# Kernel tuning notes

Measured on AMD Instinct MI355X. Metric: run time of the kernel, lower is better.

## Reference

```python
import jax, jax.numpy as jnp
import numpy as np

N_NODES = 50000
N_EDGES = 600000
IN_CH = 128
OUT_CH = 32
L1 = IN_CH - (IN_CH - OUT_CH) // 3          # 96
L2 = IN_CH - (2 * (IN_CH - OUT_CH)) // 3    # 64


def _lin(key, fan_in, fan_out):
    bound = 1.0 / np.sqrt(fan_in)
    return jax.random.uniform(key, (fan_in, fan_out), jnp.float32, -bound, bound)


def setup_inputs() -> dict:
    key = jax.random.key(0)
    ks = jax.random.split(key, 12)
    x = jax.random.normal(ks[0], (N_NODES, IN_CH), jnp.float32)
    edge_index = jax.random.randint(ks[1], (2, N_EDGES), 0, N_NODES, jnp.int64 if jax.config.jax_enable_x64 else jnp.int32)
    return {
        "x": x,
        "edge_index": edge_index,
        "w1_rel": _lin(ks[2], IN_CH, L1),
        "w1_root": _lin(ks[3], IN_CH, L1),
        "b1": jnp.zeros((L1,), jnp.float32),
        "w2_rel": _lin(ks[4], L1, L2),
        "w2_root": _lin(ks[5], L1, L2),
        "b2": jnp.zeros((L2,), jnp.float32),
        "w_mu": _lin(ks[6], L2, OUT_CH),
        "b_mu": jnp.zeros((OUT_CH,), jnp.float32),
        "w_ls": _lin(ks[7], L2, OUT_CH),
        "b_ls": jnp.zeros((OUT_CH,), jnp.float32),
    }


def reference(x, edge_index, w1_rel, w1_root, b1, w2_rel, w2_root, b2,
              w_mu, b_mu, w_ls, b_ls):
    src, dst = edge_index[0], edge_index[1]

    # PyG GraphConv (aggr='add'): out_i = W_rel @ sum_{j->i} x_j + W_root @ x_i + b
    def graph_conv(h, wr, wroot, b):
        agg = jax.ops.segment_sum(h[src], dst, num_segments=N_NODES)
        return agg @ wr + h @ wroot + b

    h = jax.nn.relu(graph_conv(x, w1_rel, w1_root, b1))
    h = jax.nn.relu(graph_conv(h, w2_rel, w2_root, b2))

    # GCNConv: add self-loops, symmetric deg^-1/2 normalization (shared by mu / logstd)
    loops = jnp.arange(N_NODES, dtype=src.dtype)
    src_sl = jnp.concatenate([src, loops])
    dst_sl = jnp.concatenate([dst, loops])
    deg = jax.ops.segment_sum(jnp.ones_like(dst_sl, h.dtype), dst_sl, num_segments=N_NODES)
    dinv = jnp.where(deg > 0, jax.lax.rsqrt(deg), 0.0)
    norm = dinv[src_sl] * dinv[dst_sl]  # [E+N]

    def gcn(h, w, b):
        m = (h @ w)[src_sl] * norm[:, None]
        return jax.ops.segment_sum(m, dst_sl, num_segments=N_NODES) + b

    return gcn(h, w_mu, b_mu), gcn(h, w_ls, b_ls)
```

## Files before the change

kernel.cpp:

```cpp
#include <hip/hip_runtime.h>
#include <cstddef>

static constexpr int NN = 50000;
static constexpr int NE = 600000;
static constexpr int NB = (NN + 255) / 256;

using f32x4 = __attribute__((ext_vector_type(4))) float;
using s16x8 = __attribute__((ext_vector_type(8))) short;

__device__ inline float bf2f(unsigned short u) {
    return __uint_as_float(((unsigned)u) << 16);
}
__device__ inline unsigned short f2bf(float f) {
    unsigned u = __float_as_uint(f);
    unsigned r = u + 0x7fffu + ((u >> 16) & 1u);
    return (unsigned short)(r >> 16);
}
__device__ inline float lof(unsigned u) { return __uint_as_float(u << 16); }
__device__ inline float hif(unsigned u) { return __uint_as_float(u & 0xffff0000u); }
__device__ inline unsigned packbf(float a, float b) {
    return (unsigned)f2bf(a) | ((unsigned)f2bf(b) << 16);
}

__global__ __launch_bounds__(256)
void zero_deg_k(int* __restrict__ deg) {
    int i = blockIdx.x * 256 + threadIdx.x;
    if (i < NN) deg[i] = 0;
}

__global__ __launch_bounds__(256)
void count_deg_k(const int* __restrict__ dstv, int* __restrict__ deg) {
    int e = blockIdx.x * 256 + threadIdx.x;
    if (e < NE) atomicAdd(&deg[dstv[e]], 1);
}

__global__ __launch_bounds__(256)
void scan_reduce_k(const int* __restrict__ deg, int* __restrict__ partial) {
    __shared__ int buf[256];
    int i = blockIdx.x * 256 + threadIdx.x;
    buf[threadIdx.x] = (i < NN) ? deg[i] : 0;
    __syncthreads();
    #pragma unroll
    for (int off = 128; off > 0; off >>= 1) {
        if (threadIdx.x < off) buf[threadIdx.x] += buf[threadIdx.x + off];
        __syncthreads();
    }
    if (threadIdx.x == 0) partial[blockIdx.x] = buf[0];
}

__global__ __launch_bounds__(256)
void scan_partials_k(int* __restrict__ partial, int* __restrict__ row_start) {
    __shared__ int buf[256];
    int t = threadIdx.x;
    int v = (t < NB) ? partial[t] : 0;
    buf[t] = v;
    __syncthreads();
    #pragma unroll
    for (int off = 1; off < 256; off <<= 1) {
        int tv = (t >= off) ? buf[t - off] : 0;
        __syncthreads();
        buf[t] += tv;
        __syncthreads();
    }
    if (t < NB) partial[t] = buf[t] - v;
    if (t == 255) row_start[NN] = buf[255];
}

__global__ __launch_bounds__(256)
void scan_final_k(const int* __restrict__ deg, const int* __restrict__ partial,
                  int* __restrict__ row_start, int* __restrict__ cursor,
                  float* __restrict__ dinv) {
    __shared__ int buf[256];
    int i = blockIdx.x * 256 + threadIdx.x;
    int t = threadIdx.x;
    int v = (i < NN) ? deg[i] : 0;
    buf[t] = v;
    __syncthreads();
    #pragma unroll
    for (int off = 1; off < 256; off <<= 1) {
        int tv = (t >= off) ? buf[t - off] : 0;
        __syncthreads();
        buf[t] += tv;
        __syncthreads();
    }
    if (i < NN) {
        int pos = partial[blockIdx.x] + buf[t] - v;
        row_start[i] = pos;
        cursor[i] = pos;
        dinv[i] = rsqrtf((float)v + 1.0f);
    }
}

__global__ __launch_bounds__(256)
void fill_k(const int* __restrict__ srcv, const int* __restrict__ dstv,
            int* __restrict__ cursor, int* __restrict__ csr)
{
    int e = blockIdx.x * 256 + threadIdx.x;
    if (e < NE) {
        int pos = atomicAdd(&cursor[dstv[e]], 1);
        csr[pos] = srcv[e];
    }
}

__global__ __launch_bounds__(256)
void wprep_k(const float* __restrict__ w1_rel, const float* __restrict__ w1_root,
             const float* __restrict__ w2_rel, const float* __restrict__ w2_root,
             const float* __restrict__ w_mu,   const float* __restrict__ w_ls,
             unsigned short* __restrict__ wt1, unsigned short* __restrict__ wt2,
             unsigned short* __restrict__ wt3)
{
    int i = blockIdx.x * 256 + threadIdx.x;
    if (i < 24576) {
        int k = i / 192, n = i % 192;
        float v = (n < 96) ? w1_rel[k * 96 + n] : w1_root[k * 96 + (n - 96)];
        wt1[n * 128 + k] = f2bf(v);
    } else if (i < 36864) {
        int j = i - 24576;
        int k = j / 128, n = j % 128;
        float v = (n < 64) ? w2_rel[k * 64 + n] : w2_root[k * 64 + (n - 64)];
        wt2[n * 96 + k] = f2bf(v);
    } else if (i < 40960) {
        int j = i - 36864;
        int k = j / 64, n = j % 64;
        float v = (n < 32) ? w_mu[k * 32 + n] : w_ls[k * 32 + (n - 32)];
        wt3[n * 64 + k] = f2bf(v);
    }
}

template<int K, int NH, bool XB, bool SCALE>
__global__ __launch_bounds__(256)
void gemm_mfma(const void* __restrict__ Xv,
               const unsigned short* __restrict__ WT,
               const float* __restrict__ biasB,
               const float* __restrict__ scale,
               unsigned short* __restrict__ out0,
               unsigned short* __restrict__ out1)
{
    constexpr int KQ = K / 4;
    constexpr int PB = K * 2;
    constexpr int KS = K / 32;
    constexpr int NT = NH / 16;
    __shared__ short lds[(128 + NH) * K];
    char* ldsb = (char*)lds;
    const int tid = threadIdx.x;
    const int blk = blockIdx.x;
    const int half = blockIdx.y;

    const unsigned short* wt = WT + (size_t)half * NH * K;
    unsigned short* outp = half ? out1 : out0;

    #pragma unroll
    for (int it = 0; it < KQ / 2; ++it) {
        int idx = it * 256 + tid;
        int r = idx / KQ, c4 = idx % KQ;
        int node = blk * 128 + r; if (node >= NN) node = NN - 1;
        uint2 p;
        if (XB) {
            p = *(const uint2*)((const unsigned short*)Xv + (size_t)node * K + c4 * 4);
        } else {
            float4 v = *(const float4*)((const float*)Xv + (size_t)node * K + c4 * 4);
            p.x = packbf(v.x, v.y); p.y = packbf(v.z, v.w);
        }
        unsigned byte = (unsigned)(r * PB + c4 * 8) ^ ((unsigned)(r & 7) << 4);
        *(uint2*)(ldsb + byte) = p;
    }
    #pragma unroll
    for (int it = 0; it < NH * KQ / 256; ++it) {
        int idx = it * 256 + tid;
        int n = idx / KQ, c4 = idx % KQ;
        uint2 p = *(const uint2*)(wt + (size_t)n * K + c4 * 4);
        int pr = 128 + n;
        unsigned byte = (unsigned)(pr * PB + c4 * 8) ^ ((unsigned)(pr & 7) << 4);
        *(uint2*)(ldsb + byte) = p;
    }
    __syncthreads();

    const int wv = tid >> 6, lane = tid & 63;
    const int r15 = lane & 15, g = lane >> 4;

    s16x8 afr[2][KS];
    #pragma unroll
    for (int ms = 0; ms < 2; ++ms) {
        #pragma unroll
        for (int ks = 0; ks < KS; ++ks) {
            int r = wv * 32 + ms * 16 + r15;
            unsigned byte = (unsigned)(r * PB + ks * 64 + g * 16) ^ ((unsigned)(r & 7) << 4);
            afr[ms][ks] = *(const s16x8*)(ldsb + byte);
        }
    }

    #pragma unroll
    for (int nt = 0; nt < NT; ++nt) {
        s16x8 bfr[KS];
        #pragma unroll
        for (int ks = 0; ks < KS; ++ks) {
            int pr = 128 + nt * 16 + r15;
            unsigned byte = (unsigned)(pr * PB + ks * 64 + g * 16) ^ ((unsigned)(pr & 7) << 4);
            bfr[ks] = *(const s16x8*)(ldsb + byte);
        }
        int c = nt * 16 + r15;
        float bias = (half && biasB) ? biasB[c] : 0.f;
        #pragma unroll
        for (int ms = 0; ms < 2; ++ms) {
            f32x4 acc = {0.f, 0.f, 0.f, 0.f};
            #pragma unroll
            for (int ks = 0; ks < KS; ++ks)
                acc = __builtin_amdgcn_mfma_f32_16x16x32_bf16(afr[ms][ks], bfr[ks], acc, 0, 0, 0);
            int nb = blk * 128 + wv * 32 + ms * 16 + g * 4;
            #pragma unroll
            for (int rg = 0; rg < 4; ++rg) {
                int node = nb + rg;
                if (node < NN) {
                    float v = acc[rg] + bias;
                    if (SCALE) v *= scale[node];
                    outp[(size_t)node * NH + c] = f2bf(v);
                }
            }
        }
    }
}

template<int OC>
__global__ __launch_bounds__(256)
void gather_relu_k(const int* __restrict__ row_start,
                   const int* __restrict__ csr,
                   const unsigned short* __restrict__ msg,
                   unsigned short* __restrict__ hio)
{
    constexpr int G = OC / 8;
    int idx = blockIdx.x * 256 + threadIdx.x;
    if (idx >= NN * G) return;
    int i  = idx / G;
    int c8 = (idx - i * G) * 8;
    const size_t ro = (size_t)i * OC + c8;
    float a[8];
    {
        uint4 h = *(const uint4*)&hio[ro];
        a[0] = lof(h.x); a[1] = hif(h.x); a[2] = lof(h.y); a[3] = hif(h.y);
        a[4] = lof(h.z); a[5] = hif(h.z); a[6] = lof(h.w); a[7] = hif(h.w);
    }
    int e0 = row_start[i], e1 = row_start[i + 1];
    int e = e0;
    for (; e + 2 <= e1; e += 2) {
        int s0 = csr[e], s1 = csr[e + 1];
        uint4 v0 = *(const uint4*)&msg[(size_t)s0 * OC + c8];
        uint4 v1 = *(const uint4*)&msg[(size_t)s1 * OC + c8];
        a[0] += lof(v0.x); a[1] += hif(v0.x); a[2] += lof(v0.y); a[3] += hif(v0.y);
        a[4] += lof(v0.z); a[5] += hif(v0.z); a[6] += lof(v0.w); a[7] += hif(v0.w);
        a[0] += lof(v1.x); a[1] += hif(v1.x); a[2] += lof(v1.y); a[3] += hif(v1.y);
        a[4] += lof(v1.z); a[5] += hif(v1.z); a[6] += lof(v1.w); a[7] += hif(v1.w);
    }
    if (e < e1) {
        int s = csr[e];
        uint4 v = *(const uint4*)&msg[(size_t)s * OC + c8];
        a[0] += lof(v.x); a[1] += hif(v.x); a[2] += lof(v.y); a[3] += hif(v.y);
        a[4] += lof(v.z); a[5] += hif(v.z); a[6] += lof(v.w); a[7] += hif(v.w);
    }
    uint4 o;
    o.x = packbf(fmaxf(a[0], 0.f), fmaxf(a[1], 0.f));
    o.y = packbf(fmaxf(a[2], 0.f), fmaxf(a[3], 0.f));
    o.z = packbf(fmaxf(a[4], 0.f), fmaxf(a[5], 0.f));
    o.w = packbf(fmaxf(a[6], 0.f), fmaxf(a[7], 0.f));
    *(uint4*)&hio[ro] = o;
}

__global__ __launch_bounds__(256)
void gather_gcn_k(const int* __restrict__ row_start,
                  const int* __restrict__ csr,
                  const unsigned short* __restrict__ y,
                  const float* __restrict__ dinv,
                  const float* __restrict__ b_mu,
                  const float* __restrict__ b_ls,
                  float* __restrict__ out)
{
    int idx = blockIdx.x * 256 + threadIdx.x;
    if (idx >= NN * 8) return;
    int i  = idx >> 3;
    int c8 = (idx & 7) * 8;
    float a[8];
    {
        uint4 h = *(const uint4*)&y[(size_t)i * 64 + c8];
        a[0] = lof(h.x); a[1] = hif(h.x); a[2] = lof(h.y); a[3] = hif(h.y);
        a[4] = lof(h.z); a[5] = hif(h.z); a[6] = lof(h.w); a[7] = hif(h.w);
    }
    int e0 = row_start[i], e1 = row_start[i + 1];
    int e = e0;
    for (; e + 2 <= e1; e += 2) {
        int s0 = csr[e], s1 = csr[e + 1];
        uint4 v0 = *(const uint4*)&y[(size_t)s0 * 64 + c8];
        uint4 v1 = *(const uint4*)&y[(size_t)s1 * 64 + c8];
        a[0] += lof(v0.x); a[1] += hif(v0.x); a[2] += lof(v0.y); a[3] += hif(v0.y);
        a[4] += lof(v0.z); a[5] += hif(v0.z); a[6] += lof(v0.w); a[7] += hif(v0.w);
        a[0] += lof(v1.x); a[1] += hif(v1.x); a[2] += lof(v1.y); a[3] += hif(v1.y);
        a[4] += lof(v1.z); a[5] += hif(v1.z); a[6] += lof(v1.w); a[7] += hif(v1.w);
    }
    if (e < e1) {
        int s = csr[e];
        uint4 v = *(const uint4*)&y[(size_t)s * 64 + c8];
        a[0] += lof(v.x); a[1] += hif(v.x); a[2] += lof(v.y); a[3] += hif(v.y);
        a[4] += lof(v.z); a[5] += hif(v.z); a[6] += lof(v.w); a[7] += hif(v.w);
    }
    float di = dinv[i];
    const float* b;
    float* o;
    if (c8 < 32) { b = &b_mu[c8];      o = &out[(size_t)i * 32 + c8]; }
    else         { b = &b_ls[c8 - 32]; o = &out[(size_t)NN * 32 + (size_t)i * 32 + (c8 - 32)]; }
    float4 r0, r1;
    r0.x = di * a[0] + b[0]; r0.y = di * a[1] + b[1];
    r0.z = di * a[2] + b[2]; r0.w = di * a[3] + b[3];
    r1.x = di * a[4] + b[4]; r1.y = di * a[5] + b[5];
    r1.z = di * a[6] + b[6]; r1.w = di * a[7] + b[7];
    *(float4*)&o[0] = r0;
    *(float4*)&o[4] = r1;
}

extern "C" void kernel_launch(void* const* d_in, const int* in_sizes, int n_in,
                              void* d_out, int out_size, void* d_ws, size_t ws_size,
                              hipStream_t stream)
{
    (void)in_sizes; (void)n_in; (void)out_size; (void)ws_size;
    const float* x       = (const float*)d_in[0];
    const int*   ei      = (const int*)d_in[1];
    const int*   srcv    = ei;
    const int*   dstv    = ei + NE;
    const float* w1_rel  = (const float*)d_in[2];
    const float* w1_root = (const float*)d_in[3];
    const float* b1      = (const float*)d_in[4];
    const float* w2_rel  = (const float*)d_in[5];
    const float* w2_root = (const float*)d_in[6];
    const float* b2      = (const float*)d_in[7];
    const float* w_mu    = (const float*)d_in[8];
    const float* b_mu    = (const float*)d_in[9];
    const float* w_ls    = (const float*)d_in[10];
    const float* b_ls    = (const float*)d_in[11];
    float* out = (float*)d_out;

    char* ws = (char*)d_ws;
    unsigned short* t1 = (unsigned short*)(ws);
    unsigned short* h1 = (unsigned short*)(ws + 9600000);
    unsigned short* t2 = (unsigned short*)(ws + 19200000);
    unsigned short* h2 = (unsigned short*)(ws + 25600000);
    unsigned short* y  = (unsigned short*)(ws + 32000000);
    int* csr       = (int*)(ws + 38400000);
    int* row_start = (int*)(ws + 40800000);
    int* cursor    = (int*)(ws + 41000016);
    float* dinv    = (float*)(ws + 41200016);
    int* deg       = (int*)(ws + 41400016);
    int* partial   = (int*)(ws + 41600016);
    unsigned short* wt1 = (unsigned short*)(ws + 41700016);
    unsigned short* wt2 = (unsigned short*)(ws + 41749168);
    unsigned short* wt3 = (unsigned short*)(ws + 41773744);

    zero_deg_k<<<NB, 256, 0, stream>>>(deg);
    wprep_k<<<160, 256, 0, stream>>>(w1_rel, w1_root, w2_rel, w2_root, w_mu, w_ls,
                                     wt1, wt2, wt3);
    count_deg_k<<<(NE + 255) / 256, 256, 0, stream>>>(dstv, deg);
    scan_reduce_k<<<NB, 256, 0, stream>>>(deg, partial);
    scan_partials_k<<<1, 256, 0, stream>>>(partial, row_start);
    scan_final_k<<<NB, 256, 0, stream>>>(deg, partial, row_start, cursor, dinv);
    fill_k<<<(NE + 255) / 256, 256, 0, stream>>>(srcv, dstv, cursor, csr);

    const int NGB = (NN + 127) / 128;

    gemm_mfma<128, 96, false, false><<<dim3(NGB, 2), 256, 0, stream>>>(
        x, wt1, b1, nullptr, t1, h1);
    gather_relu_k<96><<<(NN * 12 + 255) / 256, 256, 0, stream>>>(row_start, csr, t1, h1);

    gemm_mfma<96, 64, true, false><<<dim3(NGB, 2), 256, 0, stream>>>(
        h1, wt2, b2, nullptr, t2, h2);
    gather_relu_k<64><<<(NN * 8 + 255) / 256, 256, 0, stream>>>(row_start, csr, t2, h2);

    gemm_mfma<64, 64, true, true><<<dim3(NGB, 1), 256, 0, stream>>>(
        h2, wt3, nullptr, dinv, y, nullptr);
    gather_gcn_k<<<(NN * 8 + 255) / 256, 256, 0, stream>>>(row_start, csr, y, dinv, b_mu, b_ls, out);
}
```

Measured before the change: 178.6 us.

## Fuse neighbor gather+ReLU into following GEMM and merge preprocessing kernels

Each layer's CSR gather, root-term add and ReLU now runs inside the next layer's MFMA GEMM kernel. The activated 64-node tile is written straight to LDS instead of round-tripping h1/h2 through global memory, which removes two kernels and the intermediate writes and reads. The degree zeroing is merged with weight prep, and the partial-sum scan is folded into the final scan kernel, cutting launches. In exchange, the gather's irregular latency now sits inside the GEMM blocks, with fewer threads per node-feature and more LDS per block.

```diff
diff --git a/kernel.cpp b/kernel.cpp
--- a/kernel.cpp
+++ b/kernel.cpp
@@ -23,93 +23,15 @@
 }
 
 __global__ __launch_bounds__(256)
-void zero_deg_k(int* __restrict__ deg) {
+void zero_wprep_k(int* __restrict__ deg,
+                  const float* __restrict__ w1_rel, const float* __restrict__ w1_root,
+                  const float* __restrict__ w2_rel, const float* __restrict__ w2_root,
+                  const float* __restrict__ w_mu,   const float* __restrict__ w_ls,
+                  unsigned short* __restrict__ wt1, unsigned short* __restrict__ wt2,
+                  unsigned short* __restrict__ wt3)
+{
     int i = blockIdx.x * 256 + threadIdx.x;
     if (i < NN) deg[i] = 0;
-}
-
-__global__ __launch_bounds__(256)
-void count_deg_k(const int* __restrict__ dstv, int* __restrict__ deg) {
-    int e = blockIdx.x * 256 + threadIdx.x;
-    if (e < NE) atomicAdd(&deg[dstv[e]], 1);
-}
-
-__global__ __launch_bounds__(256)
-void scan_reduce_k(const int* __restrict__ deg, int* __restrict__ partial) {
-    __shared__ int buf[256];
-    int i = blockIdx.x * 256 + threadIdx.x;
-    buf[threadIdx.x] = (i < NN) ? deg[i] : 0;
-    __syncthreads();
-    #pragma unroll
-    for (int off = 128; off > 0; off >>= 1) {
-        if (threadIdx.x < off) buf[threadIdx.x] += buf[threadIdx.x + off];
-        __syncthreads();
-    }
-    if (threadIdx.x == 0) partial[blockIdx.x] = buf[0];
-}
-
-__global__ __launch_bounds__(256)
-void scan_partials_k(int* __restrict__ partial, int* __restrict__ row_start) {
-    __shared__ int buf[256];
-    int t = threadIdx.x;
-    int v = (t < NB) ? partial[t] : 0;
-    buf[t] = v;
-    __syncthreads();
-    #pragma unroll
-    for (int off = 1; off < 256; off <<= 1) {
-        int tv = (t >= off) ? buf[t - off] : 0;
-        __syncthreads();
-        buf[t] += tv;
-        __syncthreads();
-    }
-    if (t < NB) partial[t] = buf[t] - v;
-    if (t == 255) row_start[NN] = buf[255];
-}
-
-__global__ __launch_bounds__(256)
-void scan_final_k(const int* __restrict__ deg, const int* __restrict__ partial,
-                  int* __restrict__ row_start, int* __restrict__ cursor,
-                  float* __restrict__ dinv) {
-    __shared__ int buf[256];
-    int i = blockIdx.x * 256 + threadIdx.x;
-    int t = threadIdx.x;
-    int v = (i < NN) ? deg[i] : 0;
-    buf[t] = v;
-    __syncthreads();
-    #pragma unroll
-    for (int off = 1; off < 256; off <<= 1) {
-        int tv = (t >= off) ? buf[t - off] : 0;
-        __syncthreads();
-        buf[t] += tv;
-        __syncthreads();
-    }
-    if (i < NN) {
-        int pos = partial[blockIdx.x] + buf[t] - v;
-        row_start[i] = pos;
-        cursor[i] = pos;
-        dinv[i] = rsqrtf((float)v + 1.0f);
-    }
-}
-
-__global__ __launch_bounds__(256)
-void fill_k(const int* __restrict__ srcv, const int* __restrict__ dstv,
-            int* __restrict__ cursor, int* __restrict__ csr)
-{
-    int e = blockIdx.x * 256 + threadIdx.x;
-    if (e < NE) {
-        int pos = atomicAdd(&cursor[dstv[e]], 1);
-        csr[pos] = srcv[e];
-    }
-}
-
-__global__ __launch_bounds__(256)
-void wprep_k(const float* __restrict__ w1_rel, const float* __restrict__ w1_root,
-             const float* __restrict__ w2_rel, const float* __restrict__ w2_root,
-             const float* __restrict__ w_mu,   const float* __restrict__ w_ls,
-             unsigned short* __restrict__ wt1, unsigned short* __restrict__ wt2,
-             unsigned short* __restrict__ wt3)
-{
-    int i = blockIdx.x * 256 + threadIdx.x;
     if (i < 24576) {
         int k = i / 192, n = i % 192;
         float v = (n < 96) ? w1_rel[k * 96 + n] : w1_root[k * 96 + (n - 96)];
@@ -124,6 +46,74 @@
         int k = j / 64, n = j % 64;
         float v = (n < 32) ? w_mu[k * 32 + n] : w_ls[k * 32 + (n - 32)];
         wt3[n * 64 + k] = f2bf(v);
+    }
+}
+
+__global__ __launch_bounds__(256)
+void count_deg_k(const int* __restrict__ dstv, int* __restrict__ deg) {
+    int e = blockIdx.x * 256 + threadIdx.x;
+    if (e < NE) atomicAdd(&deg[dstv[e]], 1);
+}
+
+__global__ __launch_bounds__(256)
+void scan_reduce_k(const int* __restrict__ deg, int* __restrict__ partial) {
+    __shared__ int buf[256];
+    int i = blockIdx.x * 256 + threadIdx.x;
+    buf[threadIdx.x] = (i < NN) ? deg[i] : 0;
+    __syncthreads();
+    #pragma unroll
+    for (int off = 128; off > 0; off >>= 1) {
+        if (threadIdx.x < off) buf[threadIdx.x] += buf[threadIdx.x + off];
+        __syncthreads();
+    }
+    if (threadIdx.x == 0) partial[blockIdx.x] = buf[0];
+}
+
+__global__ __launch_bounds__(256)
+void scan_final2_k(const int* __restrict__ deg, const int* __restrict__ partial,
+                   int* __restrict__ row_start, int* __restrict__ cursor,
+                   float* __restrict__ dinv) {
+    __shared__ int pb[256], po[256], buf[256];
+    int t = threadIdx.x;
+    int pv = (t < NB) ? partial[t] : 0;
+    pb[t] = pv; po[t] = pv;
+    __syncthreads();
+    #pragma unroll
+    for (int off = 1; off < 256; off <<= 1) {
+        int tv = (t >= off) ? pb[t - off] : 0;
+        __syncthreads();
+        pb[t] += tv;
+        __syncthreads();
+    }
+    int i = blockIdx.x * 256 + t;
+    int v = (i < NN) ? deg[i] : 0;
+    buf[t] = v;
+    __syncthreads();
+    #pragma unroll
+    for (int off = 1; off < 256; off <<= 1) {
+        int tv = (t >= off) ? buf[t - off] : 0;
+        __syncthreads();
+        buf[t] += tv;
+        __syncthreads();
+    }
+    int blkoff = pb[blockIdx.x] - po[blockIdx.x];
+    if (i < NN) {
+        int pos = blkoff + buf[t] - v;
+        row_start[i] = pos;
+        cursor[i] = pos;
+        dinv[i] = rsqrtf((float)v + 1.0f);
+    }
+    if (blockIdx.x == 0 && t == 0) row_start[NN] = pb[NB - 1];
+}
+
+__global__ __launch_bounds__(256)
+void fill_k(const int* __restrict__ srcv, const int* __restrict__ dstv,
+            int* __restrict__ cursor, int* __restrict__ csr)
+{
+    int e = blockIdx.x * 256 + threadIdx.x;
+    if (e < NE) {
+        int pos = atomicAdd(&cursor[dstv[e]], 1);
+        csr[pos] = srcv[e];
     }
 }
 
@@ -220,48 +210,118 @@
     }
 }
 
-template<int OC>
-__global__ __launch_bounds__(256)
-void gather_relu_k(const int* __restrict__ row_start,
+template<int K, int NHT, bool SPLIT, bool SCALE>
+__global__ __launch_bounds__(256)
+void gather_gemm_k(const int* __restrict__ row_start,
                    const int* __restrict__ csr,
                    const unsigned short* __restrict__ msg,
-                   unsigned short* __restrict__ hio)
-{
-    constexpr int G = OC / 8;
-    int idx = blockIdx.x * 256 + threadIdx.x;
-    if (idx >= NN * G) return;
-    int i  = idx / G;
-    int c8 = (idx - i * G) * 8;
-    const size_t ro = (size_t)i * OC + c8;
-    float a[8];
-    {
-        uint4 h = *(const uint4*)&hio[ro];
-        a[0] = lof(h.x); a[1] = hif(h.x); a[2] = lof(h.y); a[3] = hif(h.y);
-        a[4] = lof(h.z); a[5] = hif(h.z); a[6] = lof(h.w); a[7] = hif(h.w);
-    }
-    int e0 = row_start[i], e1 = row_start[i + 1];
-    int e = e0;
-    for (; e + 2 <= e1; e += 2) {
-        int s0 = csr[e], s1 = csr[e + 1];
-        uint4 v0 = *(const uint4*)&msg[(size_t)s0 * OC + c8];
-        uint4 v1 = *(const uint4*)&msg[(size_t)s1 * OC + c8];
-        a[0] += lof(v0.x); a[1] += hif(v0.x); a[2] += lof(v0.y); a[3] += hif(v0.y);
-        a[4] += lof(v0.z); a[5] += hif(v0.z); a[6] += lof(v0.w); a[7] += hif(v0.w);
-        a[0] += lof(v1.x); a[1] += hif(v1.x); a[2] += lof(v1.y); a[3] += hif(v1.y);
-        a[4] += lof(v1.z); a[5] += hif(v1.z); a[6] += lof(v1.w); a[7] += hif(v1.w);
-    }
-    if (e < e1) {
-        int s = csr[e];
-        uint4 v = *(const uint4*)&msg[(size_t)s * OC + c8];
-        a[0] += lof(v.x); a[1] += hif(v.x); a[2] += lof(v.y); a[3] += hif(v.y);
-        a[4] += lof(v.z); a[5] += hif(v.z); a[6] += lof(v.w); a[7] += hif(v.w);
-    }
-    uint4 o;
-    o.x = packbf(fmaxf(a[0], 0.f), fmaxf(a[1], 0.f));
-    o.y = packbf(fmaxf(a[2], 0.f), fmaxf(a[3], 0.f));
-    o.z = packbf(fmaxf(a[4], 0.f), fmaxf(a[5], 0.f));
-    o.w = packbf(fmaxf(a[6], 0.f), fmaxf(a[7], 0.f));
-    *(uint4*)&hio[ro] = o;
+                   const unsigned short* __restrict__ hpre,
+                   const unsigned short* __restrict__ WT,
+                   const float* __restrict__ biasHi,
+                   const float* __restrict__ scale,
+                   unsigned short* __restrict__ out0,
+                   unsigned short* __restrict__ out1)
+{
+    constexpr int G   = K / 8;
+    constexpr int KQ  = K / 4;
+    constexpr int PB  = K * 2;
+    constexpr int KS  = K / 32;
+    constexpr int NT  = NHT / 16;
+    constexpr int NHh = NHT / 2;
+    __shared__ short lds[(64 + NHT) * K];
+    char* ldsb = (char*)lds;
+    const int tid = threadIdx.x;
+    const int blk = blockIdx.x;
+
+    for (int w = tid; w < 64 * G; w += 256) {
+        int r = w / G, ch = w - r * G;
+        int c8 = ch * 8;
+        int node = blk * 64 + r;
+        float a[8] = {0.f,0.f,0.f,0.f,0.f,0.f,0.f,0.f};
+        if (node < NN) {
+            uint4 h = *(const uint4*)&hpre[(size_t)node * K + c8];
+            a[0] = lof(h.x); a[1] = hif(h.x); a[2] = lof(h.y); a[3] = hif(h.y);
+            a[4] = lof(h.z); a[5] = hif(h.z); a[6] = lof(h.w); a[7] = hif(h.w);
+            int e0 = row_start[node], e1 = row_start[node + 1];
+            int e = e0;
+            for (; e + 2 <= e1; e += 2) {
+                int s0 = csr[e], s1 = csr[e + 1];
+                uint4 v0 = *(const uint4*)&msg[(size_t)s0 * K + c8];
+                uint4 v1 = *(const uint4*)&msg[(size_t)s1 * K + c8];
+                a[0] += lof(v0.x); a[1] += hif(v0.x); a[2] += lof(v0.y); a[3] += hif(v0.y);
+                a[4] += lof(v0.z); a[5] += hif(v0.z); a[6] += lof(v0.w); a[7] += hif(v0.w);
+                a[0] += lof(v1.x); a[1] += hif(v1.x); a[2] += lof(v1.y); a[3] += hif(v1.y);
+                a[4] += lof(v1.z); a[5] += hif(v1.z); a[6] += lof(v1.w); a[7] += hif(v1.w);
+            }
+            if (e < e1) {
+                int s = csr[e];
+                uint4 v = *(const uint4*)&msg[(size_t)s * K + c8];
+                a[0] += lof(v.x); a[1] += hif(v.x); a[2] += lof(v.y); a[3] += hif(v.y);
+                a[4] += lof(v.z); a[5] += hif(v.z); a[6] += lof(v.w); a[7] += hif(v.w);
+            }
+            #pragma unroll
+            for (int q = 0; q < 8; ++q) a[q] = fmaxf(a[q], 0.f);
+        }
+        uint4 o;
+        o.x = packbf(a[0], a[1]); o.y = packbf(a[2], a[3]);
+        o.z = packbf(a[4], a[5]); o.w = packbf(a[6], a[7]);
+        unsigned byte = (unsigned)(r * PB + ch * 16) ^ ((unsigned)(r & 7) << 4);
+        *(uint4*)(ldsb + byte) = o;
+    }
+    #pragma unroll
+    for (int it = 0; it < NHT * KQ / 256; ++it) {
+        int idx = it * 256 + tid;
+        int n = idx / KQ, c4 = idx % KQ;
+        uint2 p = *(const uint2*)(WT + (size_t)n * K + c4 * 4);
+        int pr = 64 + n;
+        unsigned byte = (unsigned)(pr * PB + c4 * 8) ^ ((unsigned)(pr & 7) << 4);
+        *(uint2*)(ldsb + byte) = p;
+    }
+    __syncthreads();
+
+    const int wv = tid >> 6, lane = tid & 63;
+    const int r15 = lane & 15, g = lane >> 4;
+
+    s16x8 afr[KS];
+    #pragma unroll
+    for (int ks = 0; ks < KS; ++ks) {
+        int r = wv * 16 + r15;
+        unsigned byte = (unsigned)(r * PB + ks * 64 + g * 16) ^ ((unsigned)(r & 7) << 4);
+        afr[ks] = *(const s16x8*)(ldsb + byte);
+    }
+
+    #pragma unroll
+    for (int nt = 0; nt < NT; ++nt) {
+        s16x8 bfr[KS];
+        #pragma unroll
+        for (int ks = 0; ks < KS; ++ks) {
+            int pr = 64 + nt * 16 + r15;
+            unsigned byte = (unsigned)(pr * PB + ks * 64 + g * 16) ^ ((unsigned)(pr & 7) << 4);
+            bfr[ks] = *(const s16x8*)(ldsb + byte);
+        }
+        int c = nt * 16 + r15;
+        float bias = 0.f;
+        if (SPLIT && biasHi && c >= NHh) bias = biasHi[c - NHh];
+        f32x4 acc = {0.f, 0.f, 0.f, 0.f};
+        #pragma unroll
+        for (int ks = 0; ks < KS; ++ks)
+            acc = __builtin_amdgcn_mfma_f32_16x16x32_bf16(afr[ks], bfr[ks], acc, 0, 0, 0);
+        int nb = blk * 64 + wv * 16 + g * 4;
+        #pragma unroll
+        for (int rg = 0; rg < 4; ++rg) {
+            int node = nb + rg;
+            if (node < NN) {
+                float v = acc[rg] + bias;
+                if (SCALE) v *= scale[node];
+                if (SPLIT) {
+                    if (c < NHh) out0[(size_t)node * NHh + c] = f2bf(v);
+                    else         out1[(size_t)node * NHh + (c - NHh)] = f2bf(v);
+                } else {
+                    out0[(size_t)node * NHT + c] = f2bf(v);
+                }
+            }
+        }
+    }
 }
 
 __global__ __launch_bounds__(256)
@@ -336,11 +396,11 @@
     float* out = (float*)d_out;
 
     char* ws = (char*)d_ws;
-    unsigned short* t1 = (unsigned short*)(ws);
-    unsigned short* h1 = (unsigned short*)(ws + 9600000);
-    unsigned short* t2 = (unsigned short*)(ws + 19200000);
-    unsigned short* h2 = (unsigned short*)(ws + 25600000);
-    unsigned short* y  = (unsigned short*)(ws + 32000000);
+    unsigned short* t1    = (unsigned short*)(ws);
+    unsigned short* h1pre = (unsigned short*)(ws + 9600000);
+    unsigned short* t2    = (unsigned short*)(ws + 19200000);
+    unsigned short* h2pre = (unsigned short*)(ws + 25600000);
+    unsigned short* y     = (unsigned short*)(ws + 32000000);
     int* csr       = (int*)(ws + 38400000);
     int* row_start = (int*)(ws + 40800000);
     int* cursor    = (int*)(ws + 41000016);
@@ -351,26 +411,21 @@
     unsigned short* wt2 = (unsigned short*)(ws + 41749168);
     unsigned short* wt3 = (unsigned short*)(ws + 41773744);
 
-    zero_deg_k<<<NB, 256, 0, stream>>>(deg);
-    wprep_k<<<160, 256, 0, stream>>>(w1_rel, w1_root, w2_rel, w2_root, w_mu, w_ls,
-                                     wt1, wt2, wt3);
+    zero_wprep_k<<<NB, 256, 0, stream>>>(deg, w1_rel, w1_root, w2_rel, w2_root,
+                                         w_mu, w_ls, wt1, wt2, wt3);
     count_deg_k<<<(NE + 255) / 256, 256, 0, stream>>>(dstv, deg);
     scan_reduce_k<<<NB, 256, 0, stream>>>(deg, partial);
-    scan_partials_k<<<1, 256, 0, stream>>>(partial, row_start);
-    scan_final_k<<<NB, 256, 0, stream>>>(deg, partial, row_start, cursor, dinv);
+    scan_final2_k<<<NB, 256, 0, stream>>>(deg, partial, row_start, cursor, dinv);
     fill_k<<<(NE + 255) / 256, 256, 0, stream>>>(srcv, dstv, cursor, csr);
 
-    const int NGB = (NN + 127) / 128;
-
-    gemm_mfma<128, 96, false, false><<<dim3(NGB, 2), 256, 0, stream>>>(
-        x, wt1, b1, nullptr, t1, h1);
-    gather_relu_k<96><<<(NN * 12 + 255) / 256, 256, 0, stream>>>(row_start, csr, t1, h1);
-
-    gemm_mfma<96, 64, true, false><<<dim3(NGB, 2), 256, 0, stream>>>(
-        h1, wt2, b2, nullptr, t2, h2);
-    gather_relu_k<64><<<(NN * 8 + 255) / 256, 256, 0, stream>>>(row_start, csr, t2, h2);
-
-    gemm_mfma<64, 64, true, true><<<dim3(NGB, 1), 256, 0, stream>>>(
-        h2, wt3, nullptr, dinv, y, nullptr);
+    gemm_mfma<128, 96, false, false><<<dim3(391, 2), 256, 0, stream>>>(
+        x, wt1, b1, nullptr, t1, h1pre);
+
+    gather_gemm_k<96, 128, true, false><<<782, 256, 0, stream>>>(
+        row_start, csr, t1, h1pre, wt2, b2, nullptr, t2, h2pre);
+
+    gather_gemm_k<64, 64, false, true><<<782, 256, 0, stream>>>(
+        row_start, csr, t2, h2pre, wt3, nullptr, dinv, y, nullptr);
+
     gather_gcn_k<<<(NN * 8 + 255) / 256, 256, 0, stream>>>(row_start, csr, y, dinv, b_mu, b_ls, out);
 }
```

Result: faster. 172.3 us (-3.5%).
